# Performance work log

Measured on AMD Instinct MI355X. Metric: run time of the kernel, lower is better.

The kernel has to match this reference:

```python
import jax, jax.numpy as jnp
import numpy as np
import math

CTX_LEN = 2048
N_EMB = 256
HEAD_SIZE = 256
N_HEADS = 8
HEAD_DIM = HEAD_SIZE // N_HEADS  # 32
B, T = 4, 2048


def setup_inputs() -> dict:
    key = jax.random.key(0)
    k1, k2, k3, k4 = jax.random.split(key, 4)
    x = jax.random.normal(k1, (B, T, N_EMB), dtype=jnp.float32)
    # torch Linear(n_emb, 3*head_size, bias=False): store as [in, out] for x @ W
    w_attn = jax.random.normal(k2, (N_EMB, 3 * HEAD_SIZE), dtype=jnp.float32) * 0.02
    pos_embs = jax.random.normal(k3, (N_HEADS, CTX_LEN, HEAD_DIM), dtype=jnp.float32) * 0.02
    w_proj = jax.random.normal(k4, (HEAD_SIZE, N_EMB), dtype=jnp.float32) * 0.02
    b_proj = jnp.zeros((N_EMB,), dtype=jnp.float32)
    return {"x": x, "w_attn": w_attn, "pos_embs": pos_embs,
            "w_proj": w_proj, "b_proj": b_proj}


def reference(x, w_attn, pos_embs, w_proj, b_proj):
    Bsz, Tlen, _ = x.shape
    qkv = x @ w_attn                               # [B,T,3*HS]
    K, Q, V = jnp.split(qkv, 3, axis=-1)           # split order: K, Q, V (as in source)
    def heads(t):                                  # [B,T,HS] -> [B,H,T,hd]
        return t.reshape(Bsz, Tlen, N_HEADS, HEAD_DIM).transpose(0, 2, 1, 3)
    K, Q, V = heads(K), heads(Q), heads(V)

    # relative position term with skew trick
    pe = pos_embs[:, -Tlen:, :]                    # [H,T,hd]
    S_rel = jnp.einsum('bhtd,hsd->bhts', Q, pe)    # [B,H,T,T]
    flip_mask = jnp.flip(jnp.tril(jnp.ones((Tlen, Tlen), dtype=x.dtype)), axis=1)
    S_rel = S_rel * flip_mask
    # pad a zero column at the front, reshape [T+1,T], drop first row -> skew
    S_rel = jnp.pad(S_rel, ((0, 0), (0, 0), (0, 0), (1, 0)))
    S_rel = S_rel.reshape(Bsz, N_HEADS, Tlen + 1, Tlen)[:, :, 1:, :]

    scores = (jnp.einsum('bhtd,bhsd->bhts', Q, K) + S_rel) / math.sqrt(HEAD_DIM)
    causal = jnp.where(jnp.tril(jnp.ones((Tlen, Tlen), dtype=bool)), 0.0, -1e9).astype(x.dtype)
    scores = scores + causal
    attn = jax.nn.softmax(scores, axis=-1)         # dropout omitted (eval mode)

    out = jnp.einsum('bhts,bhsd->bhtd', attn, V)   # [B,H,T,hd]
    out = out.transpose(0, 2, 1, 3).reshape(Bsz, Tlen, HEAD_SIZE)
    return out @ w_proj + b_proj
```

## Files before the change

### kernel.cpp

```cpp
#include <hip/hip_runtime.h>
#include <math.h>

#define BB 4
#define TT 2048
#define TTP 2112
#define NEMB 256
#define NH 8
#define HD 32

typedef __attribute__((ext_vector_type(8))) short bf8;
typedef __attribute__((ext_vector_type(4))) float f4;

static __device__ __forceinline__ unsigned short f2bf(float f) {
    union { float f; unsigned u; } v; v.f = f;
    unsigned r = v.u + 0x7FFF + ((v.u >> 16) & 1);
    return (unsigned short)(r >> 16);
}
static __device__ __forceinline__ float bf2f(unsigned short s) {
    union { unsigned u; float f; } v; v.u = ((unsigned)s) << 16;
    return v.f;
}

template <int CTRL>
static __device__ __forceinline__ float dppmv(float x) {
    return __int_as_float(__builtin_amdgcn_mov_dpp(__float_as_int(x), CTRL, 0xF, 0xF, true));
}
static __device__ __forceinline__ float rowsum16(float x) {
    x += dppmv<0xB1>(x);
    x += dppmv<0x4E>(x);
    x += dppmv<0x124>(x);
    x += dppmv<0x128>(x);
    return x;
}

static __device__ __forceinline__ void tcvt_body(const float* __restrict__ src,
                                                 unsigned short* __restrict__ dst,
                                                 int R, int C, int gx, int gy,
                                                 float (*t)[65], int tid) {
    const int c0 = gx * 64, r0 = gy * 64;
    #pragma unroll
    for (int p = 0; p < 4; ++p) {
        const int i = tid + p * 256;
        const int r = i >> 4, c4 = (i & 15) * 4;
        const float4 v = *(const float4*)(src + (long)(r0 + r) * C + c0 + c4);
        t[r][c4] = v.x; t[r][c4+1] = v.y; t[r][c4+2] = v.z; t[r][c4+3] = v.w;
    }
    __syncthreads();
    #pragma unroll
    for (int p = 0; p < 4; ++p) {
        const int i = tid + p * 256;
        const int cr = i >> 4, r4 = (i & 15) * 4;
        ushort4 vv;
        vv.x = f2bf(t[r4+0][cr]); vv.y = f2bf(t[r4+1][cr]);
        vv.z = f2bf(t[r4+2][cr]); vv.w = f2bf(t[r4+3][cr]);
        *(ushort4*)(dst + (long)(c0 + cr) * R + r0 + r4) = vv;
    }
}

__global__ __launch_bounds__(256) void prep(const float* __restrict__ pe,
                                            unsigned short* __restrict__ peb,
                                            const float* __restrict__ wa,
                                            unsigned short* __restrict__ waT,
                                            const float* __restrict__ wp,
                                            unsigned short* __restrict__ wpT) {
    __shared__ float t[64][65];
    const int bx = blockIdx.x, tid = threadIdx.x;
    if (bx < 528) {
        const int idx4 = bx * 256 + tid;
        const int h   = idx4 / 16896;
        const int rem = idx4 - h * 16896;
        const int u   = rem >> 3;
        const int d4  = (rem & 7) * 4;
        ushort4 o = make_ushort4(0, 0, 0, 0);
        if (u < TT) {
            const float4 v = *(const float4*)(pe + ((long)(h * TT + u)) * HD + d4);
            o.x = f2bf(v.x); o.y = f2bf(v.y); o.z = f2bf(v.z); o.w = f2bf(v.w);
        }
        *(ushort4*)(peb + ((long)(h * TTP + u)) * HD + d4) = o;
    } else if (bx < 576) {
        const int lo = bx - 528;
        tcvt_body(wa, waT, 256, 768, lo % 12, lo / 12, t, tid);
    } else {
        const int lo = bx - 576;
        tcvt_body(wp, wpT, 256, 256, lo % 4, lo / 4, t, tid);
    }
}

__global__ __launch_bounds__(256) void qkv_mfma(const float* __restrict__ xg,
                                                const unsigned short* __restrict__ Bg,
                                                unsigned short* __restrict__ Kb,
                                                unsigned short* __restrict__ Qb,
                                                unsigned short* __restrict__ Vt) {
    __shared__ unsigned short sm[13824];
    unsigned short* As = sm;
    unsigned short* Bs = sm + 9216;
    const int tid = threadIdx.x;
    const int wv = tid >> 6, L = tid & 63;
    const int l15 = L & 15, q = L >> 4;
    const int n0 = blockIdx.x * 64;
    const int m0 = blockIdx.y * 128;

    f4 acc[2][4];
    #pragma unroll
    for (int mt = 0; mt < 2; ++mt)
        #pragma unroll
        for (int nt = 0; nt < 4; ++nt) acc[mt][nt] = (f4){0.f,0.f,0.f,0.f};

    for (int kc = 0; kc < 4; ++kc) {
        const int k0 = kc * 64;
        __syncthreads();
        #pragma unroll
        for (int p = 0; p < 4; ++p) {
            const int i = tid + p * 256;
            const int r = i >> 3, c = i & 7;
            const float4 va = *(const float4*)(xg + (long)(m0 + r) * 256 + k0 + c * 8);
            const float4 vb = *(const float4*)(xg + (long)(m0 + r) * 256 + k0 + c * 8 + 4);
            ushort4 lo, hi;
            lo.x = f2bf(va.x); lo.y = f2bf(va.y); lo.z = f2bf(va.z); lo.w = f2bf(va.w);
            hi.x = f2bf(vb.x); hi.y = f2bf(vb.y); hi.z = f2bf(vb.z); hi.w = f2bf(vb.w);
            *(ushort4*)(As + r * 72 + c * 8)     = lo;
            *(ushort4*)(As + r * 72 + c * 8 + 4) = hi;
        }
        #pragma unroll
        for (int p = 0; p < 2; ++p) {
            const int i = tid + p * 256;
            const int r = i >> 3, c = i & 7;
            *(bf8*)(Bs + r * 72 + c * 8) = *(const bf8*)(Bg + (long)(n0 + r) * 256 + k0 + c * 8);
        }
        __syncthreads();
        #pragma unroll
        for (int kk = 0; kk < 2; ++kk) {
            const bf8 a0 = *(const bf8*)(As + (wv * 32 + l15) * 72 + kk * 32 + q * 8);
            const bf8 a1 = *(const bf8*)(As + (wv * 32 + 16 + l15) * 72 + kk * 32 + q * 8);
            #pragma unroll
            for (int nt = 0; nt < 4; ++nt) {
                const bf8 bb = *(const bf8*)(Bs + (nt * 16 + l15) * 72 + kk * 32 + q * 8);
                acc[0][nt] = __builtin_amdgcn_mfma_f32_16x16x32_bf16(a0, bb, acc[0][nt], 0, 0, 0);
                acc[1][nt] = __builtin_amdgcn_mfma_f32_16x16x32_bf16(a1, bb, acc[1][nt], 0, 0, 0);
            }
        }
    }

    const int sec = n0 >> 8;
    #pragma unroll
    for (int mt = 0; mt < 2; ++mt) {
        const int gm = m0 + wv * 32 + mt * 16 + q * 4;
        const int b = gm >> 11, tb = gm & 2047;
        #pragma unroll
        for (int nt = 0; nt < 4; ++nt) {
            const int gn = n0 + nt * 16 + l15;
            const int cc = gn & 255, h = cc >> 5, d = cc & 31;
            const long bh = (long)b * NH + h;
            const f4 a = acc[mt][nt];
            if (sec == 2) {
                ushort4 vv;
                vv.x = f2bf(a[0]); vv.y = f2bf(a[1]); vv.z = f2bf(a[2]); vv.w = f2bf(a[3]);
                *(ushort4*)(Vt + (bh * HD + d) * TT + tb) = vv;
            } else if (sec == 1) {
                #pragma unroll
                for (int r = 0; r < 4; ++r)
                    Qb[(bh * TT + tb + r) * HD + d] = f2bf(a[r] * 0.25506655788696527f);
            } else {
                #pragma unroll
                for (int r = 0; r < 4; ++r)
                    Kb[(bh * TT + tb + r) * HD + d] = f2bf(a[r]);
            }
        }
    }
}

__global__ __launch_bounds__(256) void attn_kernel(const unsigned short* __restrict__ Kb,
                                                   const unsigned short* __restrict__ Qb,
                                                   const unsigned short* __restrict__ Vtg,
                                                   const unsigned short* __restrict__ peb,
                                                   unsigned short* __restrict__ po,
                                                   float* __restrict__ pl) {
    __shared__ unsigned short lds[14592];
    unsigned short* Ks  = lds;
    unsigned short* PEs = lds + 2560;
    unsigned short* Vts = lds + 7680;
    unsigned short* Psw = lds + 9984 + (threadIdx.x >> 6) * 1152;

    const int tid = threadIdx.x;
    const int wv  = tid >> 6;
    const int L   = tid & 63;
    const int l15 = L & 15;
    const int q   = L >> 4;
    const int pair = blockIdx.x >> 1;
    const int sblk = blockIdx.x & 1;
    const int h = blockIdx.y, b = blockIdx.z;
    const long bh = (long)b * NH + h;
    const unsigned short* Kg = Kb  + bh * TT * HD;
    const unsigned short* Qg = Qb  + bh * TT * HD;
    const unsigned short* Vg = Vtg + bh * HD * TT;
    const unsigned short* Pg = peb + (long)h * TTP * HD;

    const int krow = tid >> 2, kc = tid & 3;
    const int vrow = tid >> 3, vc = tid & 7;
    const f4 z4 = {0.f, 0.f, 0.f, 0.f};
    const f4 m4 = {-16.f, -16.f, -16.f, -16.f};

    int saddr[4]; unsigned psel[4];
    #pragma unroll
    for (int r = 0; r < 4; ++r) {
        const int tcol = l15 + 15 - 4 * q - r;
        saddr[r] = ((q << 4) | (tcol & 15)) << 2;
        psel[r]  = (tcol < 16) ? 0x01000C0Cu : 0x03020C0Cu;
    }

    for (int half = 0; half < 2; ++half) {
        const int itile = half ? 31 - pair : pair;
        const int t0 = itile * 64;

        const bf8 aq = *(const bf8*)(Qg + (t0 + wv * 16 + l15) * HD + q * 8);
        f4 o0 = z4, o1 = z4;
        float l_st[4] = {0.f, 0.f, 0.f, 0.f};

        for (int jt = sblk; jt <= itile; jt += 2) {
            const int s0 = jt * 64;
            const int ubase = TT - 64 - t0 + s0;
            __syncthreads();
            *(bf8*)(Ks  + krow * 40 + kc * 8) = *(const bf8*)(Kg + (s0 + krow) * HD + kc * 8);
            *(bf8*)(Vts + vrow * 72 + vc * 8) = *(const bf8*)(Vg + vrow * TT + s0 + vc * 8);
            #pragma unroll
            for (int kk = 0; kk < 2; ++kk) {
                const int i  = tid + kk * 256;
                const int pr = i >> 2, pc = i & 3;
                *(bf8*)(PEs + pr * 40 + pc * 8) = *(const bf8*)(Pg + (long)(ubase + pr) * HD + pc * 8);
            }
            __syncthreads();

            f4 sa[4], ra[5];
            #pragma unroll
            for (int nt = 0; nt < 4; ++nt) {
                const bf8 bk = *(const bf8*)(Ks + (nt * 16 + l15) * 40 + q * 8);
                sa[nt] = __builtin_amdgcn_mfma_f32_16x16x32_bf16(aq, bk, m4, 0, 0, 0);
            }
            const int pebase = 48 - 16 * wv;
            #pragma unroll
            for (int nt = 0; nt < 5; ++nt) {
                const bf8 bp = *(const bf8*)(PEs + (pebase + nt * 16 + l15) * 40 + q * 8);
                ra[nt] = __builtin_amdgcn_mfma_f32_16x16x32_bf16(aq, bp, z4, 0, 0, 0);
            }

            #pragma unroll
            for (int nb = 0; nb < 4; ++nb) {
                #pragma unroll
                for (int r = 0; r < 4; ++r) {
                    const unsigned packed = __builtin_amdgcn_perm(
                        (unsigned)__float_as_int(ra[nb + 1][r]),
                        (unsigned)__float_as_int(ra[nb][r]), 0x07060302u);
                    const int v = __builtin_amdgcn_ds_bpermute(saddr[r], (int)packed);
                    const unsigned sel = __builtin_amdgcn_perm((unsigned)v, (unsigned)v, psel[r]);
                    sa[nb][r] += __int_as_float((int)sel);
                }
            }

            if (jt == itile) {
                #pragma unroll
                for (int nb = 0; nb < 4; ++nb)
                    #pragma unroll
                    for (int r = 0; r < 4; ++r) {
                        const int s_l = nb * 16 + l15;
                        const int t_l = wv * 16 + 4 * q + r;
                        if (s_l > t_l) sa[nb][r] = -1e30f;
                    }
            }

            #pragma unroll
            for (int r = 0; r < 4; ++r) {
                #pragma unroll
                for (int nb = 0; nb < 4; ++nb) {
                    const float p = exp2f(sa[nb][r]);
                    l_st[r] += p;
                    const unsigned pu = (unsigned)__float_as_int(p);
                    Psw[(4 * q + r) * 72 + nb * 16 + l15] =
                        (unsigned short)((pu + 0x8000u) >> 16);
                }
            }

            #pragma unroll
            for (int ks = 0; ks < 2; ++ks) {
                const bf8 ap  = *(const bf8*)(Psw + l15 * 72 + ks * 32 + q * 8);
                const bf8 bv0 = *(const bf8*)(Vts + l15 * 72 + ks * 32 + q * 8);
                const bf8 bv1 = *(const bf8*)(Vts + (16 + l15) * 72 + ks * 32 + q * 8);
                o0 = __builtin_amdgcn_mfma_f32_16x16x32_bf16(ap, bv0, o0, 0, 0, 0);
                o1 = __builtin_amdgcn_mfma_f32_16x16x32_bf16(ap, bv1, o1, 0, 0, 0);
            }
        }

        const long pt = (bh * 32 + itile) * 2 + sblk;
        unsigned short* pob = po + pt * 2048;
        #pragma unroll
        for (int r = 0; r < 4; ++r) {
            const int row = wv * 16 + 4 * q + r;
            pob[row * 32 + l15]      = f2bf(o0[r]);
            pob[row * 32 + 16 + l15] = f2bf(o1[r]);
            const float ls = rowsum16(l_st[r]);
            if (l15 == 0) pl[pt * 64 + row] = ls;
        }
    }
}

__global__ __launch_bounds__(256) void attn_merge(const unsigned short* __restrict__ po,
                                                  const float* __restrict__ pl,
                                                  unsigned short* __restrict__ attb) {
    const int i = blockIdx.x * 256 + threadIdx.x;
    const int d4   = i & 7;
    const int row  = (i >> 3) & 63;
    const int tile = (i >> 9) & 31;
    const int bh   = i >> 14;
    const int h = bh & 7, b = bh >> 3;
    const long pt0 = ((long)bh * 32 + tile) * 2;
    const float l0 = pl[pt0 * 64 + row], l1 = pl[(pt0 + 1) * 64 + row];
    const float inv = 1.0f / (l0 + l1);
    const ushort4 a = *(const ushort4*)(po + pt0 * 2048 + row * 32 + d4 * 4);
    const ushort4 c = *(const ushort4*)(po + (pt0 + 1) * 2048 + row * 32 + d4 * 4);
    ushort4 o;
    o.x = f2bf((bf2f(a.x) + bf2f(c.x)) * inv);
    o.y = f2bf((bf2f(a.y) + bf2f(c.y)) * inv);
    o.z = f2bf((bf2f(a.z) + bf2f(c.z)) * inv);
    o.w = f2bf((bf2f(a.w) + bf2f(c.w)) * inv);
    const int t = tile * 64 + row;
    *(ushort4*)(attb + ((long)(b * TT + t)) * NEMB + h * HD + d4 * 4) = o;
}

__global__ __launch_bounds__(256) void proj_mfma(const unsigned short* __restrict__ Ag,
                                                 const unsigned short* __restrict__ Bg,
                                                 const float* __restrict__ bias,
                                                 float* __restrict__ out) {
    __shared__ unsigned short sm[13824];
    unsigned short* As = sm;
    unsigned short* Bs = sm + 9216;
    const int tid = threadIdx.x;
    const int wv = tid >> 6, L = tid & 63;
    const int l15 = L & 15, q = L >> 4;
    const int n0 = blockIdx.x * 64;
    const int m0 = blockIdx.y * 128;

    f4 acc[2][4];
    #pragma unroll
    for (int mt = 0; mt < 2; ++mt)
        #pragma unroll
        for (int nt = 0; nt < 4; ++nt) acc[mt][nt] = (f4){0.f,0.f,0.f,0.f};

    for (int kc = 0; kc < 4; ++kc) {
        const int k0 = kc * 64;
        __syncthreads();
        #pragma unroll
        for (int p = 0; p < 4; ++p) {
            const int i = tid + p * 256;
            const int r = i >> 3, c = i & 7;
            *(bf8*)(As + r * 72 + c * 8) = *(const bf8*)(Ag + (long)(m0 + r) * 256 + k0 + c * 8);
        }
        #pragma unroll
        for (int p = 0; p < 2; ++p) {
            const int i = tid + p * 256;
            const int r = i >> 3, c = i & 7;
            *(bf8*)(Bs + r * 72 + c * 8) = *(const bf8*)(Bg + (long)(n0 + r) * 256 + k0 + c * 8);
        }
        __syncthreads();
        #pragma unroll
        for (int kk = 0; kk < 2; ++kk) {
            const bf8 a0 = *(const bf8*)(As + (wv * 32 + l15) * 72 + kk * 32 + q * 8);
            const bf8 a1 = *(const bf8*)(As + (wv * 32 + 16 + l15) * 72 + kk * 32 + q * 8);
            #pragma unroll
            for (int nt = 0; nt < 4; ++nt) {
                const bf8 bb = *(const bf8*)(Bs + (nt * 16 + l15) * 72 + kk * 32 + q * 8);
                acc[0][nt] = __builtin_amdgcn_mfma_f32_16x16x32_bf16(a0, bb, acc[0][nt], 0, 0, 0);
                acc[1][nt] = __builtin_amdgcn_mfma_f32_16x16x32_bf16(a1, bb, acc[1][nt], 0, 0, 0);
            }
        }
    }

    #pragma unroll
    for (int mt = 0; mt < 2; ++mt) {
        const int gm = m0 + wv * 32 + mt * 16 + q * 4;
        #pragma unroll
        for (int nt = 0; nt < 4; ++nt) {
            const int gn = n0 + nt * 16 + l15;
            const float bv = bias[gn];
            #pragma unroll
            for (int r = 0; r < 4; ++r)
                out[(long)(gm + r) * NEMB + gn] = acc[mt][nt][r] + bv;
        }
    }
}

extern "C" void kernel_launch(void* const* d_in, const int* in_sizes, int n_in,
                              void* d_out, int out_size, void* d_ws, size_t ws_size,
                              hipStream_t stream) {
    const float* x      = (const float*)d_in[0];
    const float* w_attn = (const float*)d_in[1];
    const float* pe     = (const float*)d_in[2];
    const float* w_proj = (const float*)d_in[3];
    const float* b_proj = (const float*)d_in[4];
    float* out = (float*)d_out;

    char* base = (char*)d_ws;
    unsigned short* Kb   = (unsigned short*)(base);
    unsigned short* Qb   = (unsigned short*)(base + ( 4u << 20));
    unsigned short* Vt   = (unsigned short*)(base + ( 8u << 20));
    unsigned short* attb = (unsigned short*)(base + (12u << 20));
    unsigned short* peb  = (unsigned short*)(base + (16u << 20));
    unsigned short* waT  = (unsigned short*)(base + (18u << 20));
    unsigned short* wpT  = (unsigned short*)(base + (37u << 19));
    unsigned short* po   = (unsigned short*)(base + (19u << 20));
    float*          pl   = (float*)        (base + (27u << 20));

    prep<<<dim3(592), 256, 0, stream>>>(pe, peb, w_attn, waT, w_proj, wpT);
    qkv_mfma<<<dim3(12, 64), 256, 0, stream>>>(x, waT, Kb, Qb, Vt);
    attn_kernel<<<dim3(32, NH, BB), 256, 0, stream>>>(Kb, Qb, Vt, peb, po, pl);
    attn_merge<<<dim3(2048), 256, 0, stream>>>(po, pl, attb);
    proj_mfma<<<dim3(4, 64), 256, 0, stream>>>(attb, wpT, b_proj, out);
}
```

Baseline: 153.0 us.

## Load attention operands directly from global and fuse merge into projection

Result: slower. 187.9 us (+22.8%).

```diff
diff --git a/kernel.cpp b/kernel.cpp
--- a/kernel.cpp
+++ b/kernel.cpp
@@ -175,11 +175,8 @@
                                                    const unsigned short* __restrict__ peb,
                                                    unsigned short* __restrict__ po,
                                                    float* __restrict__ pl) {
-    __shared__ unsigned short lds[14592];
-    unsigned short* Ks  = lds;
-    unsigned short* PEs = lds + 2560;
-    unsigned short* Vts = lds + 7680;
-    unsigned short* Psw = lds + 9984 + (threadIdx.x >> 6) * 1152;
+    __shared__ unsigned short Pall[4608];
+    unsigned short* Psw = Pall + (threadIdx.x >> 6) * 1152;
 
     const int tid = threadIdx.x;
     const int wv  = tid >> 6;
@@ -195,8 +192,6 @@
     const unsigned short* Vg = Vtg + bh * HD * TT;
     const unsigned short* Pg = peb + (long)h * TTP * HD;
 
-    const int krow = tid >> 2, kc = tid & 3;
-    const int vrow = tid >> 3, vc = tid & 7;
     const f4 z4 = {0.f, 0.f, 0.f, 0.f};
     const f4 m4 = {-16.f, -16.f, -16.f, -16.f};
 
@@ -207,6 +202,7 @@
         saddr[r] = ((q << 4) | (tcol & 15)) << 2;
         psel[r]  = (tcol < 16) ? 0x01000C0Cu : 0x03020C0Cu;
     }
+    const int pebase = 48 - 16 * wv;
 
     for (int half = 0; half < 2; ++half) {
         const int itile = half ? 31 - pair : pair;
@@ -218,30 +214,28 @@
 
         for (int jt = sblk; jt <= itile; jt += 2) {
             const int s0 = jt * 64;
-            const int ubase = TT - 64 - t0 + s0;
-            __syncthreads();
-            *(bf8*)(Ks  + krow * 40 + kc * 8) = *(const bf8*)(Kg + (s0 + krow) * HD + kc * 8);
-            *(bf8*)(Vts + vrow * 72 + vc * 8) = *(const bf8*)(Vg + vrow * TT + s0 + vc * 8);
-            #pragma unroll
-            for (int kk = 0; kk < 2; ++kk) {
-                const int i  = tid + kk * 256;
-                const int pr = i >> 2, pc = i & 3;
-                *(bf8*)(PEs + pr * 40 + pc * 8) = *(const bf8*)(Pg + (long)(ubase + pr) * HD + pc * 8);
-            }
-            __syncthreads();
+            const int ub = TT - 64 - t0 + s0 + pebase;
+
+            bf8 bk[4], bp[5], bva[2], bvb[2];
+            #pragma unroll
+            for (int nt = 0; nt < 4; ++nt)
+                bk[nt] = *(const bf8*)(Kg + (long)(s0 + nt * 16 + l15) * HD + q * 8);
+            #pragma unroll
+            for (int nt = 0; nt < 5; ++nt)
+                bp[nt] = *(const bf8*)(Pg + (long)(ub + nt * 16 + l15) * HD + q * 8);
+            #pragma unroll
+            for (int ks = 0; ks < 2; ++ks) {
+                bva[ks] = *(const bf8*)(Vg + (long)l15 * TT + s0 + ks * 32 + q * 8);
+                bvb[ks] = *(const bf8*)(Vg + (long)(16 + l15) * TT + s0 + ks * 32 + q * 8);
+            }
 
             f4 sa[4], ra[5];
             #pragma unroll
-            for (int nt = 0; nt < 4; ++nt) {
-                const bf8 bk = *(const bf8*)(Ks + (nt * 16 + l15) * 40 + q * 8);
-                sa[nt] = __builtin_amdgcn_mfma_f32_16x16x32_bf16(aq, bk, m4, 0, 0, 0);
-            }
-            const int pebase = 48 - 16 * wv;
-            #pragma unroll
-            for (int nt = 0; nt < 5; ++nt) {
-                const bf8 bp = *(const bf8*)(PEs + (pebase + nt * 16 + l15) * 40 + q * 8);
-                ra[nt] = __builtin_amdgcn_mfma_f32_16x16x32_bf16(aq, bp, z4, 0, 0, 0);
-            }
+            for (int nt = 0; nt < 4; ++nt)
+                sa[nt] = __builtin_amdgcn_mfma_f32_16x16x32_bf16(aq, bk[nt], m4, 0, 0, 0);
+            #pragma unroll
+            for (int nt = 0; nt < 5; ++nt)
+                ra[nt] = __builtin_amdgcn_mfma_f32_16x16x32_bf16(aq, bp[nt], z4, 0, 0, 0);
 
             #pragma unroll
             for (int nb = 0; nb < 4; ++nb) {
@@ -281,11 +275,9 @@
 
             #pragma unroll
             for (int ks = 0; ks < 2; ++ks) {
-                const bf8 ap  = *(const bf8*)(Psw + l15 * 72 + ks * 32 + q * 8);
-                const bf8 bv0 = *(const bf8*)(Vts + l15 * 72 + ks * 32 + q * 8);
-                const bf8 bv1 = *(const bf8*)(Vts + (16 + l15) * 72 + ks * 32 + q * 8);
-                o0 = __builtin_amdgcn_mfma_f32_16x16x32_bf16(ap, bv0, o0, 0, 0, 0);
-                o1 = __builtin_amdgcn_mfma_f32_16x16x32_bf16(ap, bv1, o1, 0, 0, 0);
+                const bf8 ap = *(const bf8*)(Psw + l15 * 72 + ks * 32 + q * 8);
+                o0 = __builtin_amdgcn_mfma_f32_16x16x32_bf16(ap, bva[ks], o0, 0, 0, 0);
+                o1 = __builtin_amdgcn_mfma_f32_16x16x32_bf16(ap, bvb[ks], o1, 0, 0, 0);
             }
         }
 
@@ -302,30 +294,8 @@
     }
 }
 
-__global__ __launch_bounds__(256) void attn_merge(const unsigned short* __restrict__ po,
-                                                  const float* __restrict__ pl,
-                                                  unsigned short* __restrict__ attb) {
-    const int i = blockIdx.x * 256 + threadIdx.x;
-    const int d4   = i & 7;
-    const int row  = (i >> 3) & 63;
-    const int tile = (i >> 9) & 31;
-    const int bh   = i >> 14;
-    const int h = bh & 7, b = bh >> 3;
-    const long pt0 = ((long)bh * 32 + tile) * 2;
-    const float l0 = pl[pt0 * 64 + row], l1 = pl[(pt0 + 1) * 64 + row];
-    const float inv = 1.0f / (l0 + l1);
-    const ushort4 a = *(const ushort4*)(po + pt0 * 2048 + row * 32 + d4 * 4);
-    const ushort4 c = *(const ushort4*)(po + (pt0 + 1) * 2048 + row * 32 + d4 * 4);
-    ushort4 o;
-    o.x = f2bf((bf2f(a.x) + bf2f(c.x)) * inv);
-    o.y = f2bf((bf2f(a.y) + bf2f(c.y)) * inv);
-    o.z = f2bf((bf2f(a.z) + bf2f(c.z)) * inv);
-    o.w = f2bf((bf2f(a.w) + bf2f(c.w)) * inv);
-    const int t = tile * 64 + row;
-    *(ushort4*)(attb + ((long)(b * TT + t)) * NEMB + h * HD + d4 * 4) = o;
-}
-
-__global__ __launch_bounds__(256) void proj_mfma(const unsigned short* __restrict__ Ag,
+__global__ __launch_bounds__(256) void proj_mfma(const unsigned short* __restrict__ po,
+                                                 const float* __restrict__ pl,
                                                  const unsigned short* __restrict__ Bg,
                                                  const float* __restrict__ bias,
                                                  float* __restrict__ out) {
@@ -351,7 +321,32 @@
         for (int p = 0; p < 4; ++p) {
             const int i = tid + p * 256;
             const int r = i >> 3, c = i & 7;
-            *(bf8*)(As + r * 72 + c * 8) = *(const bf8*)(Ag + (long)(m0 + r) * 256 + k0 + c * 8);
+            const int gm = m0 + r;
+            const int bloc = gm >> 11, t = gm & 2047;
+            const int k = k0 + c * 8;
+            const int hh = k >> 5, d0 = k & 31;
+            const int tile = t >> 6, row = t & 63;
+            const long pt0 = ((long)(bloc * NH + hh) * 32 + tile) * 2;
+            const float l0 = pl[pt0 * 64 + row];
+            const float l1 = pl[pt0 * 64 + 64 + row];
+            const float inv = 1.0f / (l0 + l1);
+            const unsigned short* p0 = po + pt0 * 2048 + row * 32 + d0;
+            const unsigned short* p1 = p0 + 2048;
+            const ushort4 a0 = *(const ushort4*)p0;
+            const ushort4 a1 = *(const ushort4*)(p0 + 4);
+            const ushort4 c0 = *(const ushort4*)p1;
+            const ushort4 c1 = *(const ushort4*)(p1 + 4);
+            ushort4 o0, o1;
+            o0.x = f2bf((bf2f(a0.x) + bf2f(c0.x)) * inv);
+            o0.y = f2bf((bf2f(a0.y) + bf2f(c0.y)) * inv);
+            o0.z = f2bf((bf2f(a0.z) + bf2f(c0.z)) * inv);
+            o0.w = f2bf((bf2f(a0.w) + bf2f(c0.w)) * inv);
+            o1.x = f2bf((bf2f(a1.x) + bf2f(c1.x)) * inv);
+            o1.y = f2bf((bf2f(a1.y) + bf2f(c1.y)) * inv);
+            o1.z = f2bf((bf2f(a1.z) + bf2f(c1.z)) * inv);
+            o1.w = f2bf((bf2f(a1.w) + bf2f(c1.w)) * inv);
+            *(ushort4*)(As + r * 72 + c * 8)     = o0;
+            *(ushort4*)(As + r * 72 + c * 8 + 4) = o1;
         }
         #pragma unroll
         for (int p = 0; p < 2; ++p) {
@@ -401,16 +396,14 @@
     unsigned short* Kb   = (unsigned short*)(base);
     unsigned short* Qb   = (unsigned short*)(base + ( 4u << 20));
     unsigned short* Vt   = (unsigned short*)(base + ( 8u << 20));
-    unsigned short* attb = (unsigned short*)(base + (12u << 20));
-    unsigned short* peb  = (unsigned short*)(base + (16u << 20));
-    unsigned short* waT  = (unsigned short*)(base + (18u << 20));
-    unsigned short* wpT  = (unsigned short*)(base + (37u << 19));
-    unsigned short* po   = (unsigned short*)(base + (19u << 20));
-    float*          pl   = (float*)        (base + (27u << 20));
+    unsigned short* peb  = (unsigned short*)(base + (12u << 20));
+    unsigned short* waT  = (unsigned short*)(base + (14u << 20));
+    unsigned short* wpT  = (unsigned short*)(base + (29u << 19));
+    unsigned short* po   = (unsigned short*)(base + (15u << 20));
+    float*          pl   = (float*)        (base + (23u << 20));
 
     prep<<<dim3(592), 256, 0, stream>>>(pe, peb, w_attn, waT, w_proj, wpT);
     qkv_mfma<<<dim3(12, 64), 256, 0, stream>>>(x, waT, Kb, Qb, Vt);
     attn_kernel<<<dim3(32, NH, BB), 256, 0, stream>>>(Kb, Qb, Vt, peb, po, pl);
-    attn_merge<<<dim3(2048), 256, 0, stream>>>(po, pl, attb);
-    proj_mfma<<<dim3(4, 64), 256, 0, stream>>>(attb, wpT, b_proj, out);
-}
+    proj_mfma<<<dim3(4, 64), 256, 0, stream>>>(po, pl, wpT, b_proj, out);
+}
```
